# Performance work log

Hardware: AMD Instinct MI355X
Metric: run time of the kernel (lower is better)

## Reference

```python
import jax, jax.numpy as jnp
import numpy as np

B, L, D, H = 4, 2048, 256, 8
FF = 128  # ff_intermediary_depth hard-coded in module
EPS = 1e-5


def layer_norm(x, g, b):
    mu = jnp.mean(x, axis=-1, keepdims=True)
    var = jnp.mean(jnp.square(x - mu), axis=-1, keepdims=True)
    return (x - mu) * jax.lax.rsqrt(var + EPS) * g + b


def setup_inputs() -> dict:
    key = jax.random.key(0)
    ks = jax.random.split(key, 8)
    s = 1.0 / np.sqrt(D)
    return {
        "seq": jax.random.normal(ks[0], (B, L, D), dtype=jnp.float32),
        "Wq": jax.random.normal(ks[1], (D, D * H), dtype=jnp.float32) * s,
        "Wk": jax.random.normal(ks[2], (D, D * H), dtype=jnp.float32) * s,
        "Wv": jax.random.normal(ks[3], (D, D * H), dtype=jnp.float32) * s,
        "Wo": jax.random.normal(ks[4], (D * H, D), dtype=jnp.float32) * (1.0 / np.sqrt(D * H)),
        "ln1_g": jnp.ones((D,), jnp.float32),
        "ln1_b": jnp.zeros((D,), jnp.float32),
        "W1": jax.random.normal(ks[5], (D, FF), dtype=jnp.float32) * s,
        "b1": jnp.zeros((FF,), jnp.float32),
        "W2": jax.random.normal(ks[6], (FF, D), dtype=jnp.float32) * (1.0 / np.sqrt(FF)),
        "b2": jnp.zeros((D,), jnp.float32),
        "ln2_g": jnp.ones((D,), jnp.float32),
        "ln2_b": jnp.zeros((D,), jnp.float32),
    }


def reference(seq, Wq, Wk, Wv, Wo, ln1_g, ln1_b, W1, b1, W2, b2, ln2_g, ln2_b):
    b, l, d = seq.shape
    # per-head dim equals full depth d (module quirk)
    q = (seq @ Wq).reshape(b, l, H, d)
    k = (seq @ Wk).reshape(b, l, H, d)
    v = (seq @ Wv).reshape(b, l, H, d)
    scores = jnp.einsum('bqhd,bkhd->bhqk', q, k) / jnp.sqrt(jnp.float32(d))
    a = jax.nn.softmax(scores, axis=-1)
    heads = jnp.einsum('bhqk,bkhd->bqhd', a, v).reshape(b, l, H * d)
    att_out = heads @ Wo
    x = layer_norm(seq + att_out, ln1_g, ln1_b)
    ff = jax.nn.relu(x @ W1 + b1) @ W2 + b2
    return layer_norm(x + ff, ln2_g, ln2_b)
```

## Files before the change

### kernel.cpp

```cpp
#include <hip/hip_runtime.h>


typedef unsigned short u16;
typedef unsigned int   u32;
typedef __bf16 bf16x8 __attribute__((ext_vector_type(8)));
typedef __bf16 bf16x2 __attribute__((ext_vector_type(2)));
typedef float  f32x4  __attribute__((ext_vector_type(4)));

#define MFMA(a, b, c) __builtin_amdgcn_mfma_f32_16x16x32_bf16(a, b, c, 0, 0, 0)

#if __has_builtin(__builtin_amdgcn_exp2f)
#define EXP2(x) __builtin_amdgcn_exp2f(x)
#else
#define EXP2(x) exp2f(x)
#endif

#if __has_builtin(__builtin_amdgcn_permlane16_swap) && \
    __has_builtin(__builtin_amdgcn_permlane32_swap)
#define HAS_PERMSWAP 1
#else
#define HAS_PERMSWAP 0
#endif

#define CEXP 0.09016844f

__device__ __forceinline__ float b2f(u16 h) {
  return __uint_as_float(((u32)h) << 16);
}
__device__ __forceinline__ u16 f2b(float f) {
  u32 u = __float_as_uint(f);
  u += 0x7FFFu + ((u >> 16) & 1u);
  return (u16)(u >> 16);
}
__device__ __forceinline__ u32 pkbf(float lo, float hi) {
  bf16x2 v;
  v[0] = (__bf16)lo;
  v[1] = (__bf16)hi;
  return __builtin_bit_cast(u32, v);
}
__device__ __forceinline__ bf16x8 ldb8(const u16* p) { return *(const bf16x8*)p; }

typedef const __attribute__((address_space(1))) u32* gas1_t;
typedef __attribute__((address_space(3))) u32* las3_t;
__device__ __forceinline__ void gload_lds16(const u16* g, u16* lds_base) {
  __builtin_amdgcn_global_load_lds((gas1_t)(const void*)g,
                                   (las3_t)(void*)lds_base, 16, 0, 0);
}

__device__ __forceinline__ int detect_f32(const void* seq) {
  const u32* s = (const u32*)seq;
  int cnt = 0;
  #pragma unroll
  for (int i = 0; i < 64; i++) {
    u32 e = (s[i] >> 7) & 0xFFu;
    cnt += (e >= 100u && e <= 140u) ? 1 : 0;
  }
  return cnt < 48;
}

__device__ __forceinline__ u16 ldw(const void* W, size_t idx, int isf32) {
  return isf32 ? f2b(((const float*)W)[idx]) : ((const u16*)W)[idx];
}

#if HAS_PERMSWAP
__device__ __forceinline__ bf16x8 softmax_pa(f32x4 sn0, f32x4 sn1,
                                             float& lsum) {
  float p00 = EXP2(sn0[0]), p01 = EXP2(sn0[1]);
  float p02 = EXP2(sn0[2]), p03 = EXP2(sn0[3]);
  float p10 = EXP2(sn1[0]), p11 = EXP2(sn1[1]);
  float p12 = EXP2(sn1[2]), p13 = EXP2(sn1[3]);
  lsum += ((p00 + p01) + (p02 + p03)) + ((p10 + p11) + (p12 + p13));
  u32 A0 = pkbf(p00, p01), A1 = pkbf(p02, p03);
  u32 B0 = pkbf(p10, p11), B1 = pkbf(p12, p13);
  auto ra = __builtin_amdgcn_permlane32_swap(A0, B0, false, false);
  auto rb = __builtin_amdgcn_permlane32_swap(A1, B1, false, false);
  auto sa = __builtin_amdgcn_permlane16_swap(ra[0], ra[1], false, false);
  auto sb = __builtin_amdgcn_permlane16_swap(rb[0], rb[1], false, false);
  uint4 wv;
  wv.x = sa[0];
  wv.y = sb[0];
  wv.z = sa[1];
  wv.w = sb[1];
  return __builtin_bit_cast(bf16x8, wv);
}
#endif

__global__ __launch_bounds__(256) void ingest_kernel(
    const void* __restrict__ seq, const void* __restrict__ g1,
    const void* __restrict__ be1, const void* __restrict__ b1,
    const void* __restrict__ b2v, const void* __restrict__ g2,
    const void* __restrict__ be2, u16* __restrict__ sbuf,
    u16* __restrict__ vecs) {
  int isf32 = detect_f32(seq);
  int bx = blockIdx.x, tid = threadIdx.x;
  if (bx < 2048) {
    size_t i = (size_t)bx * 1024 + tid * 4;
    if (isf32) {
      const float* sp = (const float*)seq;
      u16 o0 = f2b(sp[i]), o1 = f2b(sp[i + 1]), o2 = f2b(sp[i + 2]), o3 = f2b(sp[i + 3]);
      uint2 ov; ov.x = (u32)o0 | ((u32)o1 << 16); ov.y = (u32)o2 | ((u32)o3 << 16);
      *(uint2*)(sbuf + i) = ov;
    } else {
      *(uint2*)(sbuf + i) = ((const uint2*)seq)[i >> 2];
    }
  } else {
    int t = bx - 2048;
    const void* src; int n;
    switch (t) {
      case 0: src = g1;  n = 256; break;
      case 1: src = be1; n = 256; break;
      case 2: src = b1;  n = 128; break;
      case 3: src = b2v; n = 256; break;
      case 4: src = g2;  n = 256; break;
      default: src = be2; n = 256; break;
    }
    if (tid < n) vecs[t * 256 + tid] = ldw(src, tid, isf32);
  }
}

__global__ __launch_bounds__(256) void pack_kernel(
    const void* __restrict__ Wq, const void* __restrict__ Wk,
    const void* __restrict__ Wv, const void* __restrict__ Wo,
    const void* __restrict__ W1, const void* __restrict__ W2,
    const void* __restrict__ seq,
    u16* __restrict__ pWq, u16* __restrict__ pWk, u16* __restrict__ pWv,
    u16* __restrict__ pWo, u16* __restrict__ pW1, u16* __restrict__ pW2) {
  int isf32 = detect_f32(seq);
  const void* W; u16* P; int K, N;
  switch (blockIdx.y) {
    case 0: W = Wq; P = pWq; K = 256;  N = 2048; break;
    case 1: W = Wk; P = pWk; K = 256;  N = 2048; break;
    case 2: W = Wv; P = pWv; K = 256;  N = 2048; break;
    case 3: W = Wo; P = pWo; K = 2048; N = 256;  break;
    case 4: W = W1; P = pW1; K = 256;  N = 128;  break;
    default: W = W2; P = pW2; K = 128; N = 256;  break;
  }
  int t = blockIdx.x * 256 + threadIdx.x;
  int total = (K >> 5) * (N >> 4) * 64;
  if (t >= total) return;
  int lane = t & 63, f = t >> 6;
  int NT = N >> 4;
  int kt = f / NT, nt = f - kt * NT;
  int row0 = kt * 32 + ((lane >> 4) << 3);
  int col = nt * 16 + (lane & 15);
  u16 e[8];
  #pragma unroll
  for (int j = 0; j < 8; j++) e[j] = ldw(W, (size_t)(row0 + j) * N + col, isf32);
  uint4 u;
  u.x = (u32)e[0] | ((u32)e[1] << 16);
  u.y = (u32)e[2] | ((u32)e[3] << 16);
  u.z = (u32)e[4] | ((u32)e[5] << 16);
  u.w = (u32)e[6] | ((u32)e[7] << 16);
  *(uint4*)(P + ((size_t)f * 64 + lane) * 8) = u;
}

__global__ __launch_bounds__(256, 2) void qkv_kernel(
    const u16* __restrict__ X,
    const u16* __restrict__ pWq, const u16* __restrict__ pWk,
    const u16* __restrict__ pWv,
    u16* __restrict__ Qo, u16* __restrict__ Ko, u16* __restrict__ Vo,
    int ntbase, int hc) {
  __shared__ u16 blds[64 * 512];
  const u16* Pw = (blockIdx.z == 0) ? pWq : ((blockIdx.z == 1) ? pWk : pWv);
  u16* Out = (blockIdx.z == 0) ? Qo : ((blockIdx.z == 1) ? Ko : Vo);
  int tid = threadIdx.x, lane = tid & 63, w = tid >> 6;
  int nt0 = ntbase + blockIdx.x * 8;
  int m0 = blockIdx.y * 128 + w * 32;
  bf16x8 af[2][8];
  #pragma unroll
  for (int kt = 0; kt < 8; kt++) {
    af[0][kt] = ldb8(X + (size_t)(m0 + (lane & 15)) * 256 + kt * 32 + (lane >> 4) * 8);
    af[1][kt] = ldb8(X + (size_t)(m0 + 16 + (lane & 15)) * 256 + kt * 32 + (lane >> 4) * 8);
  }
  #pragma unroll
  for (int i = 0; i < 16; i++) {
    int fl = w + i * 4;
    int kt = fl >> 3, nt = fl & 7;
    gload_lds16(Pw + ((size_t)(kt * 128 + nt0 + nt) * 64 + lane) * 8,
                blds + (size_t)fl * 512);
  }
  asm volatile("s_waitcnt vmcnt(0)" ::: "memory");
  __syncthreads();
  f32x4 acc[2][8] = {};
  #pragma unroll
  for (int kt = 0; kt < 8; kt++) {
    const u16* bp = blds + (size_t)kt * 8 * 512 + (size_t)lane * 8;
    #pragma unroll
    for (int nt = 0; nt < 8; nt++) {
      bf16x8 b = ldb8(bp + nt * 512);
      acc[0][nt] = MFMA(af[0][kt], b, acc[0][nt]);
      acc[1][nt] = MFMA(af[1][kt], b, acc[1][nt]);
    }
  }
  int isv = (blockIdx.z == 2);
  float sc = (blockIdx.z == 0) ? CEXP : 1.0f;
  int hl = blockIdx.x >> 1;
  int dd0 = (blockIdx.x & 1) * 128;
  int m0b = blockIdx.y * 128;
  int bi = m0b >> 11, l0 = m0b & 2047;
  __syncthreads();
  if (!isv) {
    #pragma unroll
    for (int mt = 0; mt < 2; mt++)
      #pragma unroll
      for (int nt = 0; nt < 8; nt++)
        #pragma unroll
        for (int r = 0; r < 4; r++)
          blds[(w * 32 + mt * 16 + (lane >> 4) * 4 + r) * 136 + nt * 16 + (lane & 15)] =
              f2b(acc[mt][nt][r] * sc);
    __syncthreads();
    #pragma unroll
    for (int i = 0; i < 8; i++) {
      int c = tid + i * 256;
      int mloc = c >> 4, q = c & 15;
      uint4 v = *(uint4*)(blds + mloc * 136 + q * 8);
      *(uint4*)(Out + ((size_t)(bi * hc + hl) * 2048 + l0 + mloc) * 256 + dd0 + q * 8) = v;
    }
  } else {
    #pragma unroll
    for (int mt = 0; mt < 2; mt++)
      #pragma unroll
      for (int nt = 0; nt < 8; nt++)
        #pragma unroll
        for (int r = 0; r < 4; r++)
          blds[(nt * 16 + (lane & 15)) * 136 + w * 32 + mt * 16 + (lane >> 4) * 4 + r] =
              f2b(acc[mt][nt][r]);
    __syncthreads();
    #pragma unroll
    for (int i = 0; i < 8; i++) {
      int c = tid + i * 256;
      int nloc = c >> 4, q = c & 15;
      uint4 v = *(uint4*)(blds + nloc * 136 + q * 8);
      *(uint4*)(Out + ((size_t)(bi * hc + hl) * 256 + dd0 + nloc) * 2048 + l0 + q * 8) = v;
    }
  }
}

__global__ __launch_bounds__(256, 2) void attn_kernel(
    const u16* __restrict__ Q, const u16* __restrict__ K,
    const u16* __restrict__ Vt, u16* __restrict__ O, int nbh) {
  __shared__ u16 kbuf[2 * 8192];
  __shared__ u16 vbuf[2 * 8192];
#if !HAS_PERMSWAP
  __shared__ u16 plds[4 * 1280];
#endif
  int tid = threadIdx.x, lane = tid & 63, w = tid >> 6;
  int bi2 = blockIdx.x;
  int bh, qt;
  if (nbh >= 8) {
    int G = nbh >> 3;
    bh = (bi2 & 7) * G + (bi2 >> 3) % G;
    qt = bi2 / (8 * G);
  } else {
    bh = bi2 % nbh; qt = bi2 / nbh;
  }
  const u16* Qb  = Q  + (size_t)bh * 2048 * 256;
  const u16* Kb  = K  + (size_t)bh * 2048 * 256;
  const u16* Vtb = Vt + (size_t)bh * 256 * 2048;
  u16* Ob = O + (size_t)bh * 2048 * 256;
  int q0 = qt * 128 + w * 32;
  bf16x8 qf[2][8];
  #pragma unroll
  for (int qq = 0; qq < 2; qq++)
    #pragma unroll
    for (int kt = 0; kt < 8; kt++)
      qf[qq][kt] = ldb8(Qb + (size_t)(q0 + qq * 16 + (lane & 15)) * 256 +
                        kt * 32 + (lane >> 4) * 8);
  f32x4 o[2][16] = {};
  float lsum[2] = {0.f, 0.f};
#if !HAS_PERMSWAP
  u16* pl = plds + (size_t)w * 1280;
#endif

  #pragma unroll
  for (int j = 0; j < 4; j++) {
    int f = w * 4 + j;
    gload_lds16(Kb + (size_t)((f >> 3) * 16 + (lane & 15)) * 256 +
                    (f & 7) * 32 + (lane >> 4) * 8,
                kbuf + f * 512);
    gload_lds16(Vtb + (size_t)(f * 16 + (lane & 15)) * 2048 + (lane >> 4) * 8,
                vbuf + f * 512);
  }

  for (int t = 0; t < 64; t++) {
    int s0i = t * 32;
    asm volatile("s_waitcnt vmcnt(0)\ns_barrier" ::: "memory");
    if (t < 63) {
      int nb = (t + 1) & 1;
      #pragma unroll
      for (int j = 0; j < 4; j++) {
        int f = w * 4 + j;
        gload_lds16(Kb + (size_t)(s0i + 32 + (f >> 3) * 16 + (lane & 15)) * 256 +
                        (f & 7) * 32 + (lane >> 4) * 8,
                    kbuf + nb * 8192 + f * 512);
        gload_lds16(Vtb + (size_t)(f * 16 + (lane & 15)) * 2048 + s0i + 32 +
                        (lane >> 4) * 8,
                    vbuf + nb * 8192 + f * 512);
      }
    }
    const u16* kb = kbuf + (t & 1) * 8192;
    f32x4 s[2][2] = {};
    __builtin_amdgcn_s_setprio(1);
    #pragma unroll
    for (int ntk = 0; ntk < 2; ntk++)
      #pragma unroll
      for (int kt = 0; kt < 8; kt++) {
        bf16x8 a = ldb8(kb + (size_t)(ntk * 8 + kt) * 512 + lane * 8);
        s[0][ntk] = MFMA(a, qf[0][kt], s[0][ntk]);
        s[1][ntk] = MFMA(a, qf[1][kt], s[1][ntk]);
      }
    __builtin_amdgcn_s_setprio(0);
#if HAS_PERMSWAP
    bf16x8 pa0 = softmax_pa(s[0][0], s[0][1], lsum[0]);
    bf16x8 pa1 = softmax_pa(s[1][0], s[1][1], lsum[1]);
#else
    #pragma unroll
    for (int qq = 0; qq < 2; qq++)
      #pragma unroll
      for (int ntk = 0; ntk < 2; ntk++) {
        float p0 = EXP2(s[qq][ntk][0]);
        float p1 = EXP2(s[qq][ntk][1]);
        float p2 = EXP2(s[qq][ntk][2]);
        float p3 = EXP2(s[qq][ntk][3]);
        lsum[qq] += (p0 + p1) + (p2 + p3);
        uint2 pk;
        pk.x = pkbf(p0, p1);
        pk.y = pkbf(p2, p3);
        *(uint2*)(pl + (qq * 16 + (lane & 15)) * 40 + 16 * ntk + 4 * (lane >> 4)) = pk;
      }
    asm volatile("s_waitcnt lgkmcnt(0)" ::: "memory");
    bf16x8 pa0 = ldb8(pl + (lane & 15) * 40 + (lane >> 4) * 8);
    bf16x8 pa1 = ldb8(pl + (16 + (lane & 15)) * 40 + (lane >> 4) * 8);
    asm volatile("s_waitcnt lgkmcnt(0)" ::: "memory");
#endif
    const u16* vb0 = vbuf + (t & 1) * 8192;
    __builtin_amdgcn_s_setprio(1);
    #pragma unroll
    for (int nt = 0; nt < 16; nt++) {
      bf16x8 vb = ldb8(vb0 + (size_t)nt * 512 + lane * 8);
      o[0][nt] = MFMA(vb, pa0, o[0][nt]);
      o[1][nt] = MFMA(vb, pa1, o[1][nt]);
    }
    __builtin_amdgcn_s_setprio(0);
  }
  u16* el = kbuf + w * 1152;
  __syncthreads();
  #pragma unroll
  for (int qq = 0; qq < 2; qq++) {
    float l = lsum[qq];
    l += __shfl_xor(l, 16);
    l += __shfl_xor(l, 32);
    float linv = 1.0f / l;
    #pragma unroll
    for (int g = 0; g < 4; g++) {
      if (qq || g) asm volatile("s_waitcnt lgkmcnt(0)" ::: "memory");
      #pragma unroll
      for (int t2 = 0; t2 < 4; t2++) {
        int nt = g * 4 + t2;
        uint2 pk;
        pk.x = pkbf(o[qq][nt][0] * linv, o[qq][nt][1] * linv);
        pk.y = pkbf(o[qq][nt][2] * linv, o[qq][nt][3] * linv);
        *(uint2*)(el + (lane & 15) * 72 + t2 * 16 + 4 * (lane >> 4)) = pk;
      }
      asm volatile("s_waitcnt lgkmcnt(0)" ::: "memory");
      #pragma unroll
      for (int rep = 0; rep < 2; rep++) {
        int ch = lane + rep * 64;
        int row = ch >> 3, c8 = ch & 7;
        uint4 v = *(uint4*)(el + row * 72 + c8 * 8);
        *(uint4*)(Ob + (size_t)(q0 + qq * 16 + row) * 256 + g * 64 + c8 * 8) = v;
      }
    }
  }
}

__global__ __launch_bounds__(128) void accum_ln1_kernel(
    const u16* __restrict__ Oc, const u16* __restrict__ pWo,
    const u16* __restrict__ sbuf, const u16* __restrict__ vecs,
    u16* __restrict__ xout) {
  __shared__ u16 blds[2 * 32 * 512];
  int tid = threadIdx.x, lane = tid & 63, w = tid >> 6;
  int m0 = blockIdx.x * 32 + w * 16;
  int arow = m0 + (lane & 15);
  int bq = arow >> 11, lrow = arow & 2047;
  f32x4 acc[16] = {};
  #pragma unroll
  for (int i = 0; i < 16; i++) {
    int fl = w + i * 2;
    int ktg = fl >> 4, nt = fl & 15;
    gload_lds16(pWo + ((size_t)(ktg * 16 + nt) * 64 + lane) * 8,
                blds + (size_t)fl * 512);
  }
  asm volatile("s_waitcnt vmcnt(0)" ::: "memory");
  __syncthreads();
  for (int r = 0; r < 32; r++) {
    int k0 = r * 2;
    const u16* cur = blds + (size_t)(r & 1) * 16384;
    bf16x8 aA, aB;
    {
      int ktl = k0, hl = ktl >> 3;
      int d0 = (ktl & 7) * 32 + (lane >> 4) * 8;
      aA = ldb8(Oc + ((size_t)(bq * 8 + hl) * 2048 + lrow) * 256 + d0);
      ktl = k0 + 1; hl = ktl >> 3;
      d0 = (ktl & 7) * 32 + (lane >> 4) * 8;
      aB = ldb8(Oc + ((size_t)(bq * 8 + hl) * 2048 + lrow) * 256 + d0);
    }
    if (r < 31) {
      u16* nxt = blds + (size_t)((r + 1) & 1) * 16384;
      #pragma unroll
      for (int i = 0; i < 16; i++) {
        int fl = w + i * 2;
        int ktg = k0 + 2 + (fl >> 4), nt = fl & 15;
        gload_lds16(pWo + ((size_t)(ktg * 16 + nt) * 64 + lane) * 8,
                    nxt + (size_t)fl * 512);
      }
    }
    #pragma unroll
    for (int kl = 0; kl < 2; kl++) {
      bf16x8 a = kl ? aB : aA;
      const u16* bp = cur + (size_t)kl * 16 * 512 + (size_t)lane * 8;
      #pragma unroll
      for (int nt = 0; nt < 16; nt++) {
        bf16x8 b = ldb8(bp + nt * 512);
        acc[nt] = MFMA(a, b, acc[nt]);
      }
    }
    asm volatile("s_waitcnt vmcnt(0)" ::: "memory");
    __syncthreads();
  }
  int rbase = m0 + (lane >> 4) * 4;
  #pragma unroll
  for (int nt = 0; nt < 16; nt++) {
    int d = nt * 16 + (lane & 15);
    #pragma unroll
    for (int r = 0; r < 4; r++)
      acc[nt][r] += b2f(sbuf[(size_t)(rbase + r) * 256 + d]);
  }
  float mu[4], rs[4];
  #pragma unroll
  for (int r = 0; r < 4; r++) {
    float sm = 0.f;
    #pragma unroll
    for (int nt = 0; nt < 16; nt++) sm += acc[nt][r];
    sm += __shfl_xor(sm, 1); sm += __shfl_xor(sm, 2);
    sm += __shfl_xor(sm, 4); sm += __shfl_xor(sm, 8);
    mu[r] = sm * (1.0f / 256.0f);
    float v = 0.f;
    #pragma unroll
    for (int nt = 0; nt < 16; nt++) { float dd = acc[nt][r] - mu[r]; v += dd * dd; }
    v += __shfl_xor(v, 1); v += __shfl_xor(v, 2);
    v += __shfl_xor(v, 4); v += __shfl_xor(v, 8);
    rs[r] = rsqrtf(v * (1.0f / 256.0f) + 1e-5f);
  }
  #pragma unroll
  for (int nt = 0; nt < 16; nt++) {
    int d = nt * 16 + (lane & 15);
    float gg = b2f(vecs[d]), bb = b2f(vecs[256 + d]);
    #pragma unroll
    for (int r = 0; r < 4; r++)
      xout[(size_t)(rbase + r) * 256 + d] = f2b((acc[nt][r] - mu[r]) * rs[r] * gg + bb);
  }
}

__global__ __launch_bounds__(256) void accum_kernel(
    const u16* __restrict__ Oc, const u16* __restrict__ pWo,
    float* __restrict__ att_out, int kt0, int hc) {
  __shared__ u16 blds[64 * 512];
  int tid = threadIdx.x, lane = tid & 63, w = tid >> 6;
  int m0 = blockIdx.x * 64 + w * 16;
  int arow = m0 + (lane & 15);
  int bq = arow >> 11, lrow = arow & 2047;
  int ktn = hc * 8;
  f32x4 acc[16] = {};
  for (int k0 = 0; k0 < ktn; k0 += 4) {
    __syncthreads();
    #pragma unroll
    for (int i = 0; i < 16; i++) {
      int fl = w + i * 4;
      int ktg = kt0 + k0 + (fl >> 4), nt = fl & 15;
      gload_lds16(pWo + ((size_t)(ktg * 16 + nt) * 64 + lane) * 8,
                  blds + (size_t)fl * 512);
    }
    asm volatile("s_waitcnt vmcnt(0)" ::: "memory");
    __syncthreads();
    #pragma unroll
    for (int kl = 0; kl < 4; kl++) {
      int ktl = k0 + kl;
      int hl = ktl >> 3;
      int d0 = (ktl & 7) * 32 + (lane >> 4) * 8;
      bf16x8 a = ldb8(Oc + ((size_t)(bq * hc + hl) * 2048 + lrow) * 256 + d0);
      const u16* bp = blds + (size_t)kl * 16 * 512 + (size_t)lane * 8;
      #pragma unroll
      for (int nt = 0; nt < 16; nt++) {
        bf16x8 b = ldb8(bp + nt * 512);
        acc[nt] = MFMA(a, b, acc[nt]);
      }
    }
  }
  int rbase = m0 + (lane >> 4) * 4;
  #pragma unroll
  for (int nt = 0; nt < 16; nt++) {
    int d = nt * 16 + (lane & 15);
    #pragma unroll
    for (int r = 0; r < 4; r++)
      att_out[(size_t)(rbase + r) * 256 + d] += acc[nt][r];
  }
}

__global__ __launch_bounds__(256) void ln1_kernel(
    const float* __restrict__ att_out, const u16* __restrict__ sbuf,
    const u16* __restrict__ vecs, u16* __restrict__ xout) {
  int tid = threadIdx.x, lane = tid & 63, w = tid >> 6;
  int row = blockIdx.x * 4 + w;
  const float* ar = att_out + (size_t)row * 256;
  f32x4 a = *(const f32x4*)(ar + lane * 4);
  uint2 sv = *(const uint2*)(sbuf + (size_t)row * 256 + lane * 4);
  float y[4];
  y[0] = a[0] + b2f((u16)(sv.x & 0xFFFF));
  y[1] = a[1] + b2f((u16)(sv.x >> 16));
  y[2] = a[2] + b2f((u16)(sv.y & 0xFFFF));
  y[3] = a[3] + b2f((u16)(sv.y >> 16));
  float sm = y[0] + y[1] + y[2] + y[3];
  sm += __shfl_xor(sm, 1);  sm += __shfl_xor(sm, 2);  sm += __shfl_xor(sm, 4);
  sm += __shfl_xor(sm, 8);  sm += __shfl_xor(sm, 16); sm += __shfl_xor(sm, 32);
  float mu = sm * (1.0f / 256.0f);
  float v = 0.f;
  #pragma unroll
  for (int j = 0; j < 4; j++) { float d = y[j] - mu; v += d * d; }
  v += __shfl_xor(v, 1);  v += __shfl_xor(v, 2);  v += __shfl_xor(v, 4);
  v += __shfl_xor(v, 8);  v += __shfl_xor(v, 16); v += __shfl_xor(v, 32);
  float rs = rsqrtf(v * (1.0f / 256.0f) + 1e-5f);
  u16 o[4];
  #pragma unroll
  for (int j = 0; j < 4; j++) {
    int d = lane * 4 + j;
    o[j] = f2b((y[j] - mu) * rs * b2f(vecs[d]) + b2f(vecs[256 + d]));
  }
  uint2 ov; ov.x = (u32)o[0] | ((u32)o[1] << 16); ov.y = (u32)o[2] | ((u32)o[3] << 16);
  *(uint2*)(xout + (size_t)row * 256 + lane * 4) = ov;
}

__global__ __launch_bounds__(128) void ffn_ln2_kernel(
    const u16* __restrict__ x, const u16* __restrict__ pW1,
    const u16* __restrict__ pW2, const u16* __restrict__ vecs,
    const void* __restrict__ seq, void* __restrict__ out) {
  __shared__ u16 hbuf[2 * 16 * 136];
  int isf32 = detect_f32(seq);
  int tid = threadIdx.x, lane = tid & 63, w = tid >> 6;
  int m0 = blockIdx.x * 32 + w * 16;
  int arow = m0 + (lane & 15);
  u16* hb = hbuf + w * 16 * 136;
  f32x4 acc1[8] = {};
  #pragma unroll
  for (int kt = 0; kt < 8; kt++) {
    bf16x8 a = ldb8(x + (size_t)arow * 256 + kt * 32 + (lane >> 4) * 8);
    const u16* bp = pW1 + ((size_t)kt * 8 * 64 + lane) * 8;
    #pragma unroll
    for (int nt = 0; nt < 8; nt++) {
      bf16x8 b = ldb8(bp + nt * 512);
      acc1[nt] = MFMA(a, b, acc1[nt]);
    }
  }
  #pragma unroll
  for (int nt = 0; nt < 8; nt++) {
    int col = nt * 16 + (lane & 15);
    float bb = b2f(vecs[512 + col]);
    #pragma unroll
    for (int r = 0; r < 4; r++) {
      float h = fmaxf(acc1[nt][r] + bb, 0.f);
      hb[((lane >> 4) * 4 + r) * 136 + col] = f2b(h);
    }
  }
  __syncthreads();
  f32x4 acc2[16] = {};
  #pragma unroll
  for (int ks = 0; ks < 4; ks++) {
    bf16x8 a = ldb8(hb + (lane & 15) * 136 + ks * 32 + (lane >> 4) * 8);
    const u16* bp = pW2 + ((size_t)ks * 16 * 64 + lane) * 8;
    #pragma unroll
    for (int nt = 0; nt < 16; nt++) {
      bf16x8 b = ldb8(bp + nt * 512);
      acc2[nt] = MFMA(a, b, acc2[nt]);
    }
  }
  int rbase = m0 + (lane >> 4) * 4;
  #pragma unroll
  for (int nt = 0; nt < 16; nt++) {
    int d = nt * 16 + (lane & 15);
    float bb = b2f(vecs[768 + d]);
    #pragma unroll
    for (int r = 0; r < 4; r++)
      acc2[nt][r] += bb + b2f(x[(size_t)(rbase + r) * 256 + d]);
  }
  float mu[4], rs[4];
  #pragma unroll
  for (int r = 0; r < 4; r++) {
    float sm = 0.f;
    #pragma unroll
    for (int nt = 0; nt < 16; nt++) sm += acc2[nt][r];
    sm += __shfl_xor(sm, 1); sm += __shfl_xor(sm, 2);
    sm += __shfl_xor(sm, 4); sm += __shfl_xor(sm, 8);
    mu[r] = sm * (1.0f / 256.0f);
    float v = 0.f;
    #pragma unroll
    for (int nt = 0; nt < 16; nt++) { float dd = acc2[nt][r] - mu[r]; v += dd * dd; }
    v += __shfl_xor(v, 1); v += __shfl_xor(v, 2);
    v += __shfl_xor(v, 4); v += __shfl_xor(v, 8);
    rs[r] = rsqrtf(v * (1.0f / 256.0f) + 1e-5f);
  }
  #pragma unroll
  for (int nt = 0; nt < 16; nt++) {
    int d = nt * 16 + (lane & 15);
    float gg = b2f(vecs[1024 + d]), bb = b2f(vecs[1280 + d]);
    #pragma unroll
    for (int r = 0; r < 4; r++) {
      float val = (acc2[nt][r] - mu[r]) * rs[r] * gg + bb;
      size_t idx = (size_t)(rbase + r) * 256 + d;
      if (isf32) ((float*)out)[idx] = val;
      else       ((u16*)out)[idx]   = f2b(val);
    }
  }
}

__global__ __launch_bounds__(256) void sentinel_kernel(void* out, int n,
                                                       const void* seq) {
  int isf32 = detect_f32(seq);
  int i = blockIdx.x * 256 + threadIdx.x;
  if (i < n) {
    if (isf32) ((float*)out)[i] = 777.0f;
    else       ((u16*)out)[i]   = 0x4442;
  }
}

extern "C" void kernel_launch(void* const* d_in, const int* in_sizes, int n_in,
                              void* d_out, int out_size, void* d_ws, size_t ws_size,
                              hipStream_t stream) {
  (void)in_sizes; (void)n_in;
  const void* seq  = d_in[0];
  const void* Wq   = d_in[1];
  const void* Wk   = d_in[2];
  const void* Wv   = d_in[3];
  const void* Wo   = d_in[4];
  const void* g1   = d_in[5];
  const void* be1  = d_in[6];
  const void* W1   = d_in[7];
  const void* b1   = d_in[8];
  const void* W2   = d_in[9];
  const void* b2   = d_in[10];
  const void* g2   = d_in[11];
  const void* be2  = d_in[12];

  size_t o = 0;
  u16* ws = (u16*)d_ws;
  u16* pWq = ws + o; o += 524288;
  u16* pWk = ws + o; o += 524288;
  u16* pWv = ws + o; o += 524288;
  u16* pWo = ws + o; o += 524288;
  u16* pW1 = ws + o; o += 32768;
  u16* pW2 = ws + o; o += 32768;
  float* att = (float*)(ws + o); o += 4194304;
  u16* xb   = ws + o; o += 2097152;
  u16* sbuf = ws + o; o += 2097152;
  u16* vecs = ws + o; o += 2048;
  size_t fixed_elems = o;

  int hc = 0;
  for (int c = 8; c >= 1; c >>= 1) {
    size_t need = (fixed_elems + (size_t)4 * c * 2097152) * 2;
    if (need <= ws_size) { hc = c; break; }
  }
  if (hc == 0) {
    sentinel_kernel<<<dim3((out_size + 255) / 256), 256, 0, stream>>>(
        d_out, out_size, seq);
    return;
  }
  u16* Qc = ws + o; o += (size_t)hc * 2097152;
  u16* Kc = ws + o; o += (size_t)hc * 2097152;
  u16* Vc = ws + o; o += (size_t)hc * 2097152;
  u16* Oc = ws + o;

  ingest_kernel<<<dim3(2054), 256, 0, stream>>>(seq, g1, be1, b1, b2, g2, be2,
                                                sbuf, vecs);
  pack_kernel<<<dim3(256, 6), 256, 0, stream>>>(Wq, Wk, Wv, Wo, W1, W2, seq,
                                                pWq, pWk, pWv, pWo, pW1, pW2);
  if (hc == 8) {
    qkv_kernel<<<dim3(16, 64, 3), 256, 0, stream>>>(
        sbuf, pWq, pWk, pWv, Qc, Kc, Vc, 0, 8);
    attn_kernel<<<dim3(32 * 16), 256, 0, stream>>>(Qc, Kc, Vc, Oc, 32);
    accum_ln1_kernel<<<dim3(256), 128, 0, stream>>>(Oc, pWo, sbuf, vecs, xb);
  } else {
    hipMemsetAsync(att, 0, 2097152 * sizeof(float), stream);
    int nchunks = 8 / hc;
    for (int c = 0; c < nchunks; c++) {
      int nbh = 4 * hc;
      qkv_kernel<<<dim3(2 * hc, 64, 3), 256, 0, stream>>>(
          sbuf, pWq, pWk, pWv, Qc, Kc, Vc, c * hc * 16, hc);
      attn_kernel<<<dim3(nbh * 16), 256, 0, stream>>>(Qc, Kc, Vc, Oc, nbh);
      accum_kernel<<<dim3(128), 256, 0, stream>>>(Oc, pWo, att, c * hc * 8, hc);
    }
    ln1_kernel<<<dim3(2048), 256, 0, stream>>>(att, sbuf, vecs, xb);
  }
  ffn_ln2_kernel<<<dim3(256), 128, 0, stream>>>(xb, pW1, pW2, vecs, seq,
                                                (void*)d_out);
}
```

Before: 345.6 us.

## Split attention work across 8 waves of 16 query rows each

```diff
diff --git a/kernel.cpp b/kernel.cpp
--- a/kernel.cpp
+++ b/kernel.cpp
@@ -236,13 +236,13 @@
   }
 }
 
-__global__ __launch_bounds__(256, 2) void attn_kernel(
+__global__ __launch_bounds__(512, 4) void attn_kernel(
     const u16* __restrict__ Q, const u16* __restrict__ K,
     const u16* __restrict__ Vt, u16* __restrict__ O, int nbh) {
   __shared__ u16 kbuf[2 * 8192];
   __shared__ u16 vbuf[2 * 8192];
 #if !HAS_PERMSWAP
-  __shared__ u16 plds[4 * 1280];
+  __shared__ u16 plds[8 * 640];
 #endif
   int tid = threadIdx.x, lane = tid & 63, w = tid >> 6;
   int bi2 = blockIdx.x;
@@ -258,23 +258,20 @@
   const u16* Kb  = K  + (size_t)bh * 2048 * 256;
   const u16* Vtb = Vt + (size_t)bh * 256 * 2048;
   u16* Ob = O + (size_t)bh * 2048 * 256;
-  int q0 = qt * 128 + w * 32;
-  bf16x8 qf[2][8];
-  #pragma unroll
-  for (int qq = 0; qq < 2; qq++)
-    #pragma unroll
-    for (int kt = 0; kt < 8; kt++)
-      qf[qq][kt] = ldb8(Qb + (size_t)(q0 + qq * 16 + (lane & 15)) * 256 +
-                        kt * 32 + (lane >> 4) * 8);
-  f32x4 o[2][16] = {};
-  float lsum[2] = {0.f, 0.f};
+  int q0 = qt * 128 + w * 16;
+  bf16x8 qf[8];
+  #pragma unroll
+  for (int kt = 0; kt < 8; kt++)
+    qf[kt] = ldb8(Qb + (size_t)(q0 + (lane & 15)) * 256 + kt * 32 + (lane >> 4) * 8);
+  f32x4 o[16] = {};
+  float lsum = 0.f;
 #if !HAS_PERMSWAP
-  u16* pl = plds + (size_t)w * 1280;
+  u16* pl = plds + (size_t)w * 640;
 #endif
 
   #pragma unroll
-  for (int j = 0; j < 4; j++) {
-    int f = w * 4 + j;
+  for (int j = 0; j < 2; j++) {
+    int f = w * 2 + j;
     gload_lds16(Kb + (size_t)((f >> 3) * 16 + (lane & 15)) * 256 +
                     (f & 7) * 32 + (lane >> 4) * 8,
                 kbuf + f * 512);
@@ -288,8 +285,8 @@
     if (t < 63) {
       int nb = (t + 1) & 1;
       #pragma unroll
-      for (int j = 0; j < 4; j++) {
-        int f = w * 4 + j;
+      for (int j = 0; j < 2; j++) {
+        int f = w * 2 + j;
         gload_lds16(Kb + (size_t)(s0i + 32 + (f >> 3) * 16 + (lane & 15)) * 256 +
                         (f & 7) * 32 + (lane >> 4) * 8,
                     kbuf + nb * 8192 + f * 512);
@@ -299,38 +296,33 @@
       }
     }
     const u16* kb = kbuf + (t & 1) * 8192;
-    f32x4 s[2][2] = {};
+    f32x4 s[2] = {};
     __builtin_amdgcn_s_setprio(1);
     #pragma unroll
     for (int ntk = 0; ntk < 2; ntk++)
       #pragma unroll
       for (int kt = 0; kt < 8; kt++) {
         bf16x8 a = ldb8(kb + (size_t)(ntk * 8 + kt) * 512 + lane * 8);
-        s[0][ntk] = MFMA(a, qf[0][kt], s[0][ntk]);
-        s[1][ntk] = MFMA(a, qf[1][kt], s[1][ntk]);
+        s[ntk] = MFMA(a, qf[kt], s[ntk]);
       }
     __builtin_amdgcn_s_setprio(0);
 #if HAS_PERMSWAP
-    bf16x8 pa0 = softmax_pa(s[0][0], s[0][1], lsum[0]);
-    bf16x8 pa1 = softmax_pa(s[1][0], s[1][1], lsum[1]);
+    bf16x8 pa = softmax_pa(s[0], s[1], lsum);
 #else
     #pragma unroll
-    for (int qq = 0; qq < 2; qq++)
-      #pragma unroll
-      for (int ntk = 0; ntk < 2; ntk++) {
-        float p0 = EXP2(s[qq][ntk][0]);
-        float p1 = EXP2(s[qq][ntk][1]);
-        float p2 = EXP2(s[qq][ntk][2]);
-        float p3 = EXP2(s[qq][ntk][3]);
-        lsum[qq] += (p0 + p1) + (p2 + p3);
-        uint2 pk;
-        pk.x = pkbf(p0, p1);
-        pk.y = pkbf(p2, p3);
-        *(uint2*)(pl + (qq * 16 + (lane & 15)) * 40 + 16 * ntk + 4 * (lane >> 4)) = pk;
-      }
+    for (int ntk = 0; ntk < 2; ntk++) {
+      float p0 = EXP2(s[ntk][0]);
+      float p1 = EXP2(s[ntk][1]);
+      float p2 = EXP2(s[ntk][2]);
+      float p3 = EXP2(s[ntk][3]);
+      lsum += (p0 + p1) + (p2 + p3);
+      uint2 pk;
+      pk.x = pkbf(p0, p1);
+      pk.y = pkbf(p2, p3);
+      *(uint2*)(pl + (lane & 15) * 40 + 16 * ntk + 4 * (lane >> 4)) = pk;
+    }
     asm volatile("s_waitcnt lgkmcnt(0)" ::: "memory");
-    bf16x8 pa0 = ldb8(pl + (lane & 15) * 40 + (lane >> 4) * 8);
-    bf16x8 pa1 = ldb8(pl + (16 + (lane & 15)) * 40 + (lane >> 4) * 8);
+    bf16x8 pa = ldb8(pl + (lane & 15) * 40 + (lane >> 4) * 8);
     asm volatile("s_waitcnt lgkmcnt(0)" ::: "memory");
 #endif
     const u16* vb0 = vbuf + (t & 1) * 8192;
@@ -338,38 +330,34 @@
     #pragma unroll
     for (int nt = 0; nt < 16; nt++) {
       bf16x8 vb = ldb8(vb0 + (size_t)nt * 512 + lane * 8);
-      o[0][nt] = MFMA(vb, pa0, o[0][nt]);
-      o[1][nt] = MFMA(vb, pa1, o[1][nt]);
+      o[nt] = MFMA(vb, pa, o[nt]);
     }
     __builtin_amdgcn_s_setprio(0);
   }
+  float l = lsum;
+  l += __shfl_xor(l, 16);
+  l += __shfl_xor(l, 32);
+  float linv = 1.0f / l;
   u16* el = kbuf + w * 1152;
   __syncthreads();
   #pragma unroll
-  for (int qq = 0; qq < 2; qq++) {
-    float l = lsum[qq];
-    l += __shfl_xor(l, 16);
-    l += __shfl_xor(l, 32);
-    float linv = 1.0f / l;
-    #pragma unroll
-    for (int g = 0; g < 4; g++) {
-      if (qq || g) asm volatile("s_waitcnt lgkmcnt(0)" ::: "memory");
-      #pragma unroll
-      for (int t2 = 0; t2 < 4; t2++) {
-        int nt = g * 4 + t2;
-        uint2 pk;
-        pk.x = pkbf(o[qq][nt][0] * linv, o[qq][nt][1] * linv);
-        pk.y = pkbf(o[qq][nt][2] * linv, o[qq][nt][3] * linv);
-        *(uint2*)(el + (lane & 15) * 72 + t2 * 16 + 4 * (lane >> 4)) = pk;
-      }
-      asm volatile("s_waitcnt lgkmcnt(0)" ::: "memory");
-      #pragma unroll
-      for (int rep = 0; rep < 2; rep++) {
-        int ch = lane + rep * 64;
-        int row = ch >> 3, c8 = ch & 7;
-        uint4 v = *(uint4*)(el + row * 72 + c8 * 8);
-        *(uint4*)(Ob + (size_t)(q0 + qq * 16 + row) * 256 + g * 64 + c8 * 8) = v;
-      }
+  for (int g = 0; g < 4; g++) {
+    if (g) asm volatile("s_waitcnt lgkmcnt(0)" ::: "memory");
+    #pragma unroll
+    for (int t2 = 0; t2 < 4; t2++) {
+      int nt = g * 4 + t2;
+      uint2 pk;
+      pk.x = pkbf(o[nt][0] * linv, o[nt][1] * linv);
+      pk.y = pkbf(o[nt][2] * linv, o[nt][3] * linv);
+      *(uint2*)(el + (lane & 15) * 72 + t2 * 16 + 4 * (lane >> 4)) = pk;
+    }
+    asm volatile("s_waitcnt lgkmcnt(0)" ::: "memory");
+    #pragma unroll
+    for (int rep = 0; rep < 2; rep++) {
+      int ch = lane + rep * 64;
+      int row = ch >> 3, c8 = ch & 7;
+      uint4 v = *(uint4*)(el + row * 72 + c8 * 8);
+      *(uint4*)(Ob + (size_t)(q0 + row) * 256 + g * 64 + c8 * 8) = v;
     }
   }
 }
@@ -686,7 +674,7 @@
   if (hc == 8) {
     qkv_kernel<<<dim3(16, 64, 3), 256, 0, stream>>>(
         sbuf, pWq, pWk, pWv, Qc, Kc, Vc, 0, 8);
-    attn_kernel<<<dim3(32 * 16), 256, 0, stream>>>(Qc, Kc, Vc, Oc, 32);
+    attn_kernel<<<dim3(32 * 16), 512, 0, stream>>>(Qc, Kc, Vc, Oc, 32);
     accum_ln1_kernel<<<dim3(256), 128, 0, stream>>>(Oc, pWo, sbuf, vecs, xb);
   } else {
     hipMemsetAsync(att, 0, 2097152 * sizeof(float), stream);
@@ -695,7 +683,7 @@
       int nbh = 4 * hc;
       qkv_kernel<<<dim3(2 * hc, 64, 3), 256, 0, stream>>>(
           sbuf, pWq, pWk, pWv, Qc, Kc, Vc, c * hc * 16, hc);
-      attn_kernel<<<dim3(nbh * 16), 256, 0, stream>>>(Qc, Kc, Vc, Oc, nbh);
+      attn_kernel<<<dim3(nbh * 16), 512, 0, stream>>>(Qc, Kc, Vc, Oc, nbh);
       accum_kernel<<<dim3(128), 256, 0, stream>>>(Oc, pWo, att, c * hc * 8, hc);
     }
     ln1_kernel<<<dim3(2048), 256, 0, stream>>>(att, sbuf, vecs, xb);
```

After: 342.3 us. About the same (-1.0%).
